# Optimization experiments

Measured on AMD Instinct MI355X. Metric: run time of the kernel, lower is better.

Reference implementation:

```python
import jax, jax.numpy as jnp
import numpy as np

EMBED_DIM = 1024
NUM_HEADS = 16
HEAD_DIM = EMBED_DIM // NUM_HEADS


def setup_inputs() -> dict:
    key = jax.random.key(0)
    ks = jax.random.split(key, 9)
    B, S, E = 4, 2048, EMBED_DIM
    # xavier_uniform bound for square [E, E] weights
    bound = float(np.sqrt(6.0 / (E + E)))
    def w(k):
        return jax.random.uniform(k, (E, E), jnp.float32, -bound, bound)
    return {
        "x": jax.random.normal(ks[0], (B, S, E), jnp.float32),
        "Wq": w(ks[1]), "bq": jnp.zeros((E,), jnp.float32),
        "Wk": w(ks[2]), "bk": jnp.zeros((E,), jnp.float32),
        "Wv": w(ks[3]), "bv": jnp.zeros((E,), jnp.float32),
        "Wo": w(ks[4]), "bo": jnp.zeros((E,), jnp.float32),
    }


def reference(x, Wq, bq, Wk, bk, Wv, bv, Wo, bo):
    B, S, E = x.shape
    H, D = NUM_HEADS, HEAD_DIM
    # Linear projections (torch Linear: x @ W.T + b)
    q = (x @ Wq.T + bq).reshape(B, S, H, D)
    k = (x @ Wk.T + bk).reshape(B, S, H, D)
    v = (x @ Wv.T + bv).reshape(B, S, H, D)
    # per-head scaled dot-product attention (vectorized over heads)
    scores = jnp.einsum("bqhd,bkhd->bhqk", q, k) / jnp.sqrt(jnp.float32(D))
    attn = jax.nn.softmax(scores, axis=-1)
    o = jnp.einsum("bhqk,bkhd->bqhd", attn, v).reshape(B, S, E)
    return o @ Wo.T + bo
```

## Files before the change

### kernel.cpp

```cpp
#include <hip/hip_runtime.h>
#include <stdint.h>

typedef unsigned short u16;
typedef short bf16x8 __attribute__((ext_vector_type(8)));
typedef float f32x4 __attribute__((ext_vector_type(4)));

#define B_ 4
#define S_ 2048
#define H_ 16
#define D_ 64
#define E_ 1024
#define M_ (B_ * S_)

static __device__ __forceinline__ u16 f2bf(float f) {
  uint32_t u = __builtin_bit_cast(uint32_t, f);
  u += 0x7fffu + ((u >> 16) & 1u);
  return (u16)(u >> 16);
}
static __device__ __forceinline__ u16 hu16(float f) {
  return (u16)((__builtin_bit_cast(uint32_t, f) + 0x8000u) >> 16);
}
static __device__ __forceinline__ uint32_t pack2bf(float a, float b) {
  return (uint32_t)f2bf(a) | ((uint32_t)f2bf(b) << 16);
}

static __device__ __forceinline__ void gld_lds16(const void* g, void* l) {
  __builtin_amdgcn_global_load_lds(
      (const __attribute__((address_space(1))) void*)(uintptr_t)g,
      (__attribute__((address_space(3))) void*)(uint32_t)(uintptr_t)l, 16, 0, 0);
}

template <int ctrl>
static __device__ __forceinline__ float dpp_mov(float x) {
  return __builtin_bit_cast(float,
      __builtin_amdgcn_update_dpp(0, __builtin_bit_cast(int, x), ctrl, 0xF, 0xF, true));
}
static __device__ __forceinline__ float rowsum16(float x) {
  x += dpp_mov<0xB1>(x);
  x += dpp_mov<0x4E>(x);
  x += dpp_mov<0x141>(x);
  x += dpp_mov<0x140>(x);
  return x;
}

__global__ __launch_bounds__(256) void cvt_f32_bf16(const float* __restrict__ in,
                                                    u16* __restrict__ out, int n) {
  int i = (blockIdx.x * 256 + threadIdx.x) * 8;
  if (i + 8 > n) return;
  float4 a = *(const float4*)(in + i);
  float4 b = *(const float4*)(in + i + 4);
  struct __align__(16) U8 { u16 h[8]; } u;
  u.h[0] = f2bf(a.x); u.h[1] = f2bf(a.y); u.h[2] = f2bf(a.z); u.h[3] = f2bf(a.w);
  u.h[4] = f2bf(b.x); u.h[5] = f2bf(b.y); u.h[6] = f2bf(b.z); u.h[7] = f2bf(b.w);
  *(U8*)(out + i) = u;
}

template <int KIND, typename OutT>
static __device__ __forceinline__ void gemm128(const u16* __restrict__ A,
                                               const u16* __restrict__ W,
                                               const float* __restrict__ bias,
                                               OutT* __restrict__ C, int m0, int n0,
                                               float scale, u16* As, u16* Bs) {
  const int tid = threadIdx.x;
  const int wave = tid >> 6, lane = tid & 63;
  const int col16 = lane & 15, quad = lane >> 4;
  const int wm = wave >> 1, wn = wave & 1;

  f32x4 acc[4][4] = {};

  const int r0 = tid >> 3;
  const int sg8 = ((tid & 7) ^ (r0 & 7)) * 8;
  const u16* ga = A + (size_t)(m0 + r0) * E_ + sg8;
  const u16* gb = W + (size_t)(n0 + r0) * E_ + sg8;
  u16* lA = As + wave * 512;
  u16* lB = Bs + wave * 512;

  for (int k0 = 0; k0 < E_; k0 += 64) {
    __syncthreads();
#pragma unroll
    for (int i = 0; i < 4; i++) {
      gld_lds16(ga + (size_t)(i * 32) * E_ + k0, lA + i * 2048);
      gld_lds16(gb + (size_t)(i * 32) * E_ + k0, lB + i * 2048);
    }
    asm volatile("s_waitcnt vmcnt(0)" ::: "memory");
    __syncthreads();

    bf16x8 af[4][2], bw[4][2];
#pragma unroll
    for (int mt = 0; mt < 4; mt++)
#pragma unroll
      for (int ks = 0; ks < 2; ks++)
        af[mt][ks] = *(const bf16x8*)&As[(wm * 64 + mt * 16 + col16) * 64 +
                                         (((ks * 4 + quad) ^ (col16 & 7)) * 8)];
#pragma unroll
    for (int nt = 0; nt < 4; nt++)
#pragma unroll
      for (int ks = 0; ks < 2; ks++)
        bw[nt][ks] = *(const bf16x8*)&Bs[(wn * 64 + nt * 16 + col16) * 64 +
                                         (((ks * 4 + quad) ^ (col16 & 7)) * 8)];
#pragma unroll
    for (int ks = 0; ks < 2; ks++)
#pragma unroll
      for (int a = 0; a < 4; a++)
#pragma unroll
        for (int b = 0; b < 4; b++) {
          if constexpr (KIND == 2)
            acc[a][b] = __builtin_amdgcn_mfma_f32_16x16x32_bf16(af[a][ks], bw[b][ks], acc[a][b], 0, 0, 0);
          else
            acc[a][b] = __builtin_amdgcn_mfma_f32_16x16x32_bf16(bw[a][ks], af[b][ks], acc[a][b], 0, 0, 0);
        }
  }

  if constexpr (KIND == 2) {
#pragma unroll
    for (int a = 0; a < 4; a++) {
      int t = m0 + wm * 64 + a * 16 + quad * 4;
      int bb = t >> 11, s = t & (S_ - 1);
#pragma unroll
      for (int b = 0; b < 4; b++) {
        int oc = n0 + wn * 64 + b * 16 + col16;
        int h = oc >> 6, d = oc & 63;
        float bv = bias[oc];
        uint32_t lo = pack2bf(acc[a][b][0] + bv, acc[a][b][1] + bv);
        uint32_t hi = pack2bf(acc[a][b][2] + bv, acc[a][b][3] + bv);
        uint2 pk = {lo, hi};
        *(uint2*)&C[(((size_t)(bb * H_ + h) * D_ + d) * S_) + s] = pk;
      }
    }
  } else {
#pragma unroll
    for (int b = 0; b < 4; b++) {
      int row = m0 + wm * 64 + b * 16 + col16;
#pragma unroll
      for (int a = 0; a < 4; a++) {
        int nc = n0 + wn * 64 + a * 16 + quad * 4;
        float4 bv = *(const float4*)&bias[nc];
        float v0 = (acc[a][b][0] + bv.x) * scale;
        float v1 = (acc[a][b][1] + bv.y) * scale;
        float v2 = (acc[a][b][2] + bv.z) * scale;
        float v3 = (acc[a][b][3] + bv.w) * scale;
        if constexpr (KIND == 0) {
          uint2 pk = {pack2bf(v0, v1), pack2bf(v2, v3)};
          *(uint2*)&((u16*)C)[(size_t)row * E_ + nc] = pk;
        } else {
          float4 pk = {v0, v1, v2, v3};
          *(float4*)&((float*)C)[(size_t)row * E_ + nc] = pk;
        }
      }
    }
  }
}

__global__ __launch_bounds__(256) void gemm_qkv(const u16* __restrict__ xb,
                                                const u16* __restrict__ wq, const u16* __restrict__ wk,
                                                const u16* __restrict__ wv,
                                                const float* __restrict__ bq, const float* __restrict__ bk,
                                                const float* __restrict__ bv,
                                                u16* __restrict__ Qb, u16* __restrict__ Kb,
                                                u16* __restrict__ Vtb) {
  __shared__ __align__(16) u16 As[128 * 64];
  __shared__ __align__(16) u16 Bs[128 * 64];
  const int mat = blockIdx.x >> 3;
  const int n0 = (blockIdx.x & 7) * 128;
  const int m0 = blockIdx.y * 128;
  if (mat == 0)
    gemm128<0, u16>(xb, wq, bq, Qb, m0, n0, 0.125f * 1.44269504f, As, Bs);
  else if (mat == 1)
    gemm128<0, u16>(xb, wk, bk, Kb, m0, n0, 1.0f, As, Bs);
  else
    gemm128<2, u16>(xb, wv, bv, Vtb, m0, n0, 1.0f, As, Bs);
}

__global__ __launch_bounds__(256) void gemm_out(const u16* __restrict__ Ob,
                                                const u16* __restrict__ wob,
                                                const float* __restrict__ bo,
                                                float* __restrict__ out) {
  __shared__ __align__(16) u16 As[128 * 64];
  __shared__ __align__(16) u16 Bs[128 * 64];
  gemm128<1, float>(Ob, wob, bo, out, blockIdx.y * 128, blockIdx.x * 128, 1.0f, As, Bs);
}

__global__ __launch_bounds__(256) void flash_attn(const u16* __restrict__ Q,
                                                  const u16* __restrict__ K,
                                                  const u16* __restrict__ Vt,
                                                  u16* __restrict__ O) {
  __shared__ __align__(16) u16 Ks[2][64 * 64];
  __shared__ __align__(16) u16 Vs[2][64 * 64];
  __shared__ __align__(16) u16 Ps[4][32 * 72];
  const int bid = blockIdx.x;
  const int qt = bid & 15, h = (bid >> 4) & 15, b = bid >> 8;
  const int tid = threadIdx.x;
  const int wave = tid >> 6, lane = tid & 63;
  const int col16 = lane & 15, quad = lane >> 4;

  bf16x8 qf[2][2];
  const int qrow = qt * 128 + wave * 32;
#pragma unroll
  for (int mt = 0; mt < 2; mt++) {
    const u16* qp = Q + ((size_t)(b * S_ + qrow + mt * 16 + col16) * H_ + h) * D_ + quad * 8;
    qf[mt][0] = *(const bf16x8*)qp;
    qf[mt][1] = *(const bf16x8*)(qp + 32);
  }

  f32x4 o_acc[2][4] = {};
  float l_i[2][4] = {};

  const int srow = tid >> 3;
  const int sgrp = (tid & 7) ^ (srow & 7);
  const u16* Kbase = K + ((size_t)(b * S_) * H_ + h) * D_;
  const u16* Vbase = Vt + ((size_t)(b * H_ + h) * D_) * S_;
  u16* Pw = &Ps[wave][0];

  auto stage = [&](int kb, int buf) {
#pragma unroll
    for (int i = 0; i < 2; i++) {
      gld_lds16(Kbase + (size_t)(kb * 64 + i * 32 + srow) * (H_ * D_) + sgrp * 8,
                &Ks[buf][i * 2048 + wave * 512]);
      gld_lds16(Vbase + (size_t)(i * 32 + srow) * S_ + kb * 64 + sgrp * 8,
                &Vs[buf][i * 2048 + wave * 512]);
    }
  };

  stage(0, 0);
  for (int kb = 0; kb < S_ / 64; kb++) {
    const int cur = kb & 1;
    asm volatile("s_waitcnt vmcnt(0)" ::: "memory");
    __syncthreads();
    if (kb + 1 < S_ / 64) stage(kb + 1, cur ^ 1);
    const u16* KsC = Ks[cur];
    const u16* VsC = Vs[cur];

    f32x4 sacc[2][4] = {};
#pragma unroll
    for (int ks = 0; ks < 2; ks++) {
      bf16x8 kf[4];
#pragma unroll
      for (int nt = 0; nt < 4; nt++)
        kf[nt] = *(const bf16x8*)&KsC[(nt * 16 + col16) * 64 +
                                      (((ks * 4 + quad) ^ (col16 & 7)) * 8)];
#pragma unroll
      for (int mt = 0; mt < 2; mt++)
#pragma unroll
        for (int nt = 0; nt < 4; nt++)
          sacc[mt][nt] = __builtin_amdgcn_mfma_f32_16x16x32_bf16(qf[mt][ks], kf[nt], sacc[mt][nt], 0, 0, 0);
    }

#pragma unroll
    for (int mt = 0; mt < 2; mt++) {
#pragma unroll
      for (int e = 0; e < 4; e++) {
        float p0 = __builtin_amdgcn_exp2f(sacc[mt][0][e]);
        float p1 = __builtin_amdgcn_exp2f(sacc[mt][1][e]);
        float p2 = __builtin_amdgcn_exp2f(sacc[mt][2][e]);
        float p3 = __builtin_amdgcn_exp2f(sacc[mt][3][e]);
        l_i[mt][e] += (p0 + p1) + (p2 + p3);
        const int r = mt * 16 + quad * 4 + e;
        const int ro = r * 72;
        const int cb = col16 + ((r & 8) ? 16 : 0);
        Pw[ro + (cb & 63)] = hu16(p0);
        Pw[ro + ((cb + 16) & 63)] = hu16(p1);
        Pw[ro + ((cb + 32) & 63)] = hu16(p2);
        Pw[ro + ((cb + 48) & 63)] = hu16(p3);
      }
    }
    asm volatile("s_waitcnt lgkmcnt(0)" ::: "memory");

#pragma unroll
    for (int ks = 0; ks < 2; ks++) {
      bf16x8 pf[2], vf[4];
#pragma unroll
      for (int mt = 0; mt < 2; mt++)
        pf[mt] = *(const bf16x8*)&Pw[(mt * 16 + col16) * 72 +
                                     (((ks * 4 + quad + ((col16 >> 3) << 1)) & 7) * 8)];
#pragma unroll
      for (int nt = 0; nt < 4; nt++)
        vf[nt] = *(const bf16x8*)&VsC[(nt * 16 + col16) * 64 +
                                      (((ks * 4 + quad) ^ (col16 & 7)) * 8)];
#pragma unroll
      for (int mt = 0; mt < 2; mt++)
#pragma unroll
        for (int nt = 0; nt < 4; nt++)
          o_acc[mt][nt] = __builtin_amdgcn_mfma_f32_16x16x32_bf16(pf[mt], vf[nt], o_acc[mt][nt], 0, 0, 0);
    }
  }

#pragma unroll
  for (int mt = 0; mt < 2; mt++) {
#pragma unroll
    for (int e = 0; e < 4; e++) {
      float inv = 1.f / rowsum16(l_i[mt][e]);
      int s = qrow + mt * 16 + quad * 4 + e;
#pragma unroll
      for (int nt = 0; nt < 4; nt++)
        O[((size_t)(b * S_ + s) * H_ + h) * D_ + nt * 16 + col16] =
            f2bf(o_acc[mt][nt][e] * inv);
    }
  }
}

extern "C" void kernel_launch(void* const* d_in, const int* in_sizes, int n_in,
                              void* d_out, int out_size, void* d_ws, size_t ws_size,
                              hipStream_t stream) {
  (void)in_sizes; (void)n_in; (void)out_size; (void)ws_size;
  const float* x  = (const float*)d_in[0];
  const float* Wq = (const float*)d_in[1];
  const float* bq = (const float*)d_in[2];
  const float* Wk = (const float*)d_in[3];
  const float* bk = (const float*)d_in[4];
  const float* Wv = (const float*)d_in[5];
  const float* bv = (const float*)d_in[6];
  const float* Wo = (const float*)d_in[7];
  const float* bo = (const float*)d_in[8];
  float* out = (float*)d_out;

  const size_t NX = (size_t)M_ * E_;
  const size_t NW = (size_t)E_ * E_;
  u16* xb  = (u16*)d_ws;
  u16* wqb = xb + NX;
  u16* wkb = wqb + NW;
  u16* wvb = wkb + NW;
  u16* wob = wvb + NW;
  u16* Qb  = wob + NW;
  u16* Kb  = Qb + NX;
  u16* Vtb = Kb + NX;
  u16* Ob  = Vtb + NX;

  cvt_f32_bf16<<<NX / 2048, 256, 0, stream>>>(x, xb, (int)NX);
  cvt_f32_bf16<<<NW / 2048, 256, 0, stream>>>(Wq, wqb, (int)NW);
  cvt_f32_bf16<<<NW / 2048, 256, 0, stream>>>(Wk, wkb, (int)NW);
  cvt_f32_bf16<<<NW / 2048, 256, 0, stream>>>(Wv, wvb, (int)NW);
  cvt_f32_bf16<<<NW / 2048, 256, 0, stream>>>(Wo, wob, (int)NW);

  gemm_qkv<<<dim3(24, 64), 256, 0, stream>>>(xb, wqb, wkb, wvb, bq, bk, bv, Qb, Kb, Vtb);
  flash_attn<<<B_ * H_ * (S_ / 128), 256, 0, stream>>>(Qb, Kb, Vtb, Ob);
  gemm_out<<<dim3(8, 64), 256, 0, stream>>>(Ob, wob, bo, out);
}
```

Measured before the change: 304.0 us.

## Keep attention probabilities in registers via transposed 32x32 MFMA and permlane swap

Rewrites the flash-attention inner loop to compute S^T = K·Q^T with 32x32x16 MFMAs, so each lane holds one query's scores across keys. The probabilities are packed to bf16 with v_cvt_pk_bf16_f32 and rearranged with v_permlane32_swap into the A-operand layout for the PV MFMA. This drops the per-wave LDS P buffer and its write/read round trip and waitcnt. It also adds s_setprio around the MFMA groups and reduces the row sums with one cross-half shuffle. The cost is a more complex output index mapping and a dependence on gfx950-specific instructions.

```diff
diff --git a/kernel.cpp b/kernel.cpp
--- a/kernel.cpp
+++ b/kernel.cpp
@@ -4,6 +4,7 @@
 typedef unsigned short u16;
 typedef short bf16x8 __attribute__((ext_vector_type(8)));
 typedef float f32x4 __attribute__((ext_vector_type(4)));
+typedef float f32x16 __attribute__((ext_vector_type(16)));
 
 #define B_ 4
 #define S_ 2048
@@ -17,30 +18,22 @@
   u += 0x7fffu + ((u >> 16) & 1u);
   return (u16)(u >> 16);
 }
-static __device__ __forceinline__ u16 hu16(float f) {
-  return (u16)((__builtin_bit_cast(uint32_t, f) + 0x8000u) >> 16);
-}
 static __device__ __forceinline__ uint32_t pack2bf(float a, float b) {
   return (uint32_t)f2bf(a) | ((uint32_t)f2bf(b) << 16);
+}
+static __device__ __forceinline__ uint32_t cvt_pk_bf16(float a, float b) {
+  uint32_t r;
+  asm("v_cvt_pk_bf16_f32 %0, %1, %2" : "=v"(r) : "v"(a), "v"(b));
+  return r;
+}
+static __device__ __forceinline__ void pl32swap(uint32_t& a, uint32_t& b) {
+  asm volatile("v_permlane32_swap_b32 %0, %1" : "+v"(a), "+v"(b));
 }
 
 static __device__ __forceinline__ void gld_lds16(const void* g, void* l) {
   __builtin_amdgcn_global_load_lds(
       (const __attribute__((address_space(1))) void*)(uintptr_t)g,
       (__attribute__((address_space(3))) void*)(uint32_t)(uintptr_t)l, 16, 0, 0);
-}
-
-template <int ctrl>
-static __device__ __forceinline__ float dpp_mov(float x) {
-  return __builtin_bit_cast(float,
-      __builtin_amdgcn_update_dpp(0, __builtin_bit_cast(int, x), ctrl, 0xF, 0xF, true));
-}
-static __device__ __forceinline__ float rowsum16(float x) {
-  x += dpp_mov<0xB1>(x);
-  x += dpp_mov<0x4E>(x);
-  x += dpp_mov<0x141>(x);
-  x += dpp_mov<0x140>(x);
-  return x;
 }
 
 __global__ __launch_bounds__(256) void cvt_f32_bf16(const float* __restrict__ in,
@@ -186,30 +179,26 @@
                                                   u16* __restrict__ O) {
   __shared__ __align__(16) u16 Ks[2][64 * 64];
   __shared__ __align__(16) u16 Vs[2][64 * 64];
-  __shared__ __align__(16) u16 Ps[4][32 * 72];
   const int bid = blockIdx.x;
   const int qt = bid & 15, h = (bid >> 4) & 15, b = bid >> 8;
   const int tid = threadIdx.x;
   const int wave = tid >> 6, lane = tid & 63;
-  const int col16 = lane & 15, quad = lane >> 4;
-
-  bf16x8 qf[2][2];
+  const int l31 = lane & 31, hi = lane >> 5;
+  const int sw7 = l31 & 7;
+
   const int qrow = qt * 128 + wave * 32;
-#pragma unroll
-  for (int mt = 0; mt < 2; mt++) {
-    const u16* qp = Q + ((size_t)(b * S_ + qrow + mt * 16 + col16) * H_ + h) * D_ + quad * 8;
-    qf[mt][0] = *(const bf16x8*)qp;
-    qf[mt][1] = *(const bf16x8*)(qp + 32);
-  }
-
-  f32x4 o_acc[2][4] = {};
-  float l_i[2][4] = {};
+  bf16x8 qf[4];
+  const u16* qp = Q + ((size_t)(b * S_ + qrow + l31) * H_ + h) * D_ + hi * 8;
+#pragma unroll
+  for (int t = 0; t < 4; t++) qf[t] = *(const bf16x8*)(qp + t * 16);
+
+  f32x16 o_acc[2] = {};
+  float l_sum = 0.f;
 
   const int srow = tid >> 3;
   const int sgrp = (tid & 7) ^ (srow & 7);
   const u16* Kbase = K + ((size_t)(b * S_) * H_ + h) * D_;
   const u16* Vbase = Vt + ((size_t)(b * H_ + h) * D_) * S_;
-  u16* Pw = &Ps[wave][0];
 
   auto stage = [&](int kb, int buf) {
 #pragma unroll
@@ -230,71 +219,63 @@
     const u16* KsC = Ks[cur];
     const u16* VsC = Vs[cur];
 
-    f32x4 sacc[2][4] = {};
-#pragma unroll
-    for (int ks = 0; ks < 2; ks++) {
-      bf16x8 kf[4];
-#pragma unroll
-      for (int nt = 0; nt < 4; nt++)
-        kf[nt] = *(const bf16x8*)&KsC[(nt * 16 + col16) * 64 +
-                                      (((ks * 4 + quad) ^ (col16 & 7)) * 8)];
-#pragma unroll
-      for (int mt = 0; mt < 2; mt++)
-#pragma unroll
-        for (int nt = 0; nt < 4; nt++)
-          sacc[mt][nt] = __builtin_amdgcn_mfma_f32_16x16x32_bf16(qf[mt][ks], kf[nt], sacc[mt][nt], 0, 0, 0);
-    }
-
-#pragma unroll
-    for (int mt = 0; mt < 2; mt++) {
-#pragma unroll
-      for (int e = 0; e < 4; e++) {
-        float p0 = __builtin_amdgcn_exp2f(sacc[mt][0][e]);
-        float p1 = __builtin_amdgcn_exp2f(sacc[mt][1][e]);
-        float p2 = __builtin_amdgcn_exp2f(sacc[mt][2][e]);
-        float p3 = __builtin_amdgcn_exp2f(sacc[mt][3][e]);
-        l_i[mt][e] += (p0 + p1) + (p2 + p3);
-        const int r = mt * 16 + quad * 4 + e;
-        const int ro = r * 72;
-        const int cb = col16 + ((r & 8) ? 16 : 0);
-        Pw[ro + (cb & 63)] = hu16(p0);
-        Pw[ro + ((cb + 16) & 63)] = hu16(p1);
-        Pw[ro + ((cb + 32) & 63)] = hu16(p2);
-        Pw[ro + ((cb + 48) & 63)] = hu16(p3);
+#pragma unroll
+    for (int kblk = 0; kblk < 2; kblk++) {
+      const int krow = kblk * 32 + l31;
+      const int ksw = krow & 7;
+      f32x16 sacc = {};
+      __builtin_amdgcn_s_setprio(1);
+#pragma unroll
+      for (int t = 0; t < 4; t++) {
+        bf16x8 kf = *(const bf16x8*)&KsC[krow * 64 + (((2 * t + hi) ^ ksw) * 8)];
+        sacc = __builtin_amdgcn_mfma_f32_32x32x16_bf16(kf, qf[t], sacc, 0, 0, 0);
       }
-    }
-    asm volatile("s_waitcnt lgkmcnt(0)" ::: "memory");
-
-#pragma unroll
-    for (int ks = 0; ks < 2; ks++) {
-      bf16x8 pf[2], vf[4];
-#pragma unroll
-      for (int mt = 0; mt < 2; mt++)
-        pf[mt] = *(const bf16x8*)&Pw[(mt * 16 + col16) * 72 +
-                                     (((ks * 4 + quad + ((col16 >> 3) << 1)) & 7) * 8)];
-#pragma unroll
-      for (int nt = 0; nt < 4; nt++)
-        vf[nt] = *(const bf16x8*)&VsC[(nt * 16 + col16) * 64 +
-                                      (((ks * 4 + quad) ^ (col16 & 7)) * 8)];
-#pragma unroll
-      for (int mt = 0; mt < 2; mt++)
-#pragma unroll
-        for (int nt = 0; nt < 4; nt++)
-          o_acc[mt][nt] = __builtin_amdgcn_mfma_f32_16x16x32_bf16(pf[mt], vf[nt], o_acc[mt][nt], 0, 0, 0);
+      __builtin_amdgcn_s_setprio(0);
+
+      float p[16];
+#pragma unroll
+      for (int e = 0; e < 16; e++) p[e] = __builtin_amdgcn_exp2f(sacc[e]);
+      float s0 = (p[0] + p[1]) + (p[2] + p[3]);
+      float s1 = (p[4] + p[5]) + (p[6] + p[7]);
+      float s2 = (p[8] + p[9]) + (p[10] + p[11]);
+      float s3 = (p[12] + p[13]) + (p[14] + p[15]);
+      l_sum += (s0 + s1) + (s2 + s3);
+      uint32_t W[8];
+#pragma unroll
+      for (int i = 0; i < 8; i++) W[i] = cvt_pk_bf16(p[2 * i], p[2 * i + 1]);
+
+#pragma unroll
+      for (int kf2 = 0; kf2 < 2; kf2++) {
+        uint32_t w0 = W[kf2 * 4 + 0], w1 = W[kf2 * 4 + 1];
+        uint32_t w2 = W[kf2 * 4 + 2], w3 = W[kf2 * 4 + 3];
+        pl32swap(w0, w2);
+        pl32swap(w1, w3);
+        union { uint32_t w[4]; bf16x8 v; } u;
+        u.w[0] = w0; u.w[1] = w1; u.w[2] = w2; u.w[3] = w3;
+        const bf16x8 pa = u.v;
+        const int kf = kblk * 2 + kf2;
+        __builtin_amdgcn_s_setprio(1);
+#pragma unroll
+        for (int n = 0; n < 2; n++) {
+          const int dr = n * 32 + l31;
+          bf16x8 vf = *(const bf16x8*)&VsC[dr * 64 + (((2 * kf + hi) ^ sw7) * 8)];
+          o_acc[n] = __builtin_amdgcn_mfma_f32_32x32x16_bf16(pa, vf, o_acc[n], 0, 0, 0);
+        }
+        __builtin_amdgcn_s_setprio(0);
+      }
     }
   }
 
-#pragma unroll
-  for (int mt = 0; mt < 2; mt++) {
-#pragma unroll
-    for (int e = 0; e < 4; e++) {
-      float inv = 1.f / rowsum16(l_i[mt][e]);
-      int s = qrow + mt * 16 + quad * 4 + e;
-#pragma unroll
-      for (int nt = 0; nt < 4; nt++)
-        O[((size_t)(b * S_ + s) * H_ + h) * D_ + nt * 16 + col16] =
-            f2bf(o_acc[mt][nt][e] * inv);
-    }
+  float l_tot = l_sum + __shfl_xor(l_sum, 32);
+  float inv = 1.f / l_tot;
+
+#pragma unroll
+  for (int r = 0; r < 16; r++) {
+    const int ql = (r & 3) + 8 * (r >> 2) + 4 * hi;
+    const float iq = __shfl(inv, ql);
+    u16* op = O + ((size_t)(b * S_ + qrow + ql) * H_ + h) * D_ + l31;
+#pragma unroll
+    for (int n = 0; n < 2; n++) op[n * 32] = f2bf(o_acc[n][r] * iq);
   }
 }
 
```

Result: no change. 303.3 us (-0.2%).
